# Performance work log

Measured on AMD Instinct MI355X. Metric: run time of the kernel, lower is better.

Reference implementation:

```python
import jax, jax.numpy as jnp
import numpy as np

EMBED_DIM = 1024
NUM_HEADS = 16
HEAD_DIM = EMBED_DIM // NUM_HEADS


def setup_inputs() -> dict:
    key = jax.random.key(0)
    k_x, k_wqkv, k_bqkv, k_wout, k_bout = jax.random.split(key, 5)
    scale = 1.0 / np.sqrt(EMBED_DIM)
    return {
        "x": jax.random.normal(k_x, (2, 2048, EMBED_DIM), dtype=jnp.float32),
        "W_qkv": jax.random.normal(k_wqkv, (3 * EMBED_DIM, EMBED_DIM), dtype=jnp.float32) * scale,
        "b_qkv": jax.random.normal(k_bqkv, (3 * EMBED_DIM,), dtype=jnp.float32) * scale,
        "W_out": jax.random.normal(k_wout, (EMBED_DIM, EMBED_DIM), dtype=jnp.float32) * scale,
        "b_out": jax.random.normal(k_bout, (EMBED_DIM,), dtype=jnp.float32) * scale,
    }


def reference(x, W_qkv, b_qkv, W_out, b_out):
    B, L, D = x.shape
    H, hd = NUM_HEADS, HEAD_DIM
    # fused QKV projection (torch Linear: x @ W.T + b)
    qkv = x @ W_qkv.T + b_qkv                      # [B, L, 3D]
    q, k, v = jnp.split(qkv, 3, axis=-1)           # each [B, L, D]
    # [B, L, D] -> [B, H, L, hd]
    q = q.reshape(B, L, H, hd).transpose(0, 2, 1, 3)
    k = k.reshape(B, L, H, hd).transpose(0, 2, 1, 3)
    v = v.reshape(B, L, H, hd).transpose(0, 2, 1, 3)
    attn = jnp.einsum("bhqd,bhkd->bhqk", q, k) / jnp.sqrt(jnp.float32(hd))
    attn = jax.nn.softmax(attn, axis=-1)           # [B, H, L, L]
    out = jnp.einsum("bhqk,bhkd->bhqd", attn, v)   # [B, H, L, hd]
    out = out.transpose(0, 2, 1, 3).reshape(B, L, D)
    return out @ W_out.T + b_out
```

## Files before the change

kernel.cpp:

```cpp
#include <hip/hip_runtime.h>
#include <hip/hip_bf16.h>

typedef __attribute__((ext_vector_type(8))) _Float16 f16x8;
typedef __attribute__((ext_vector_type(4))) _Float16 f16x4;
typedef __attribute__((ext_vector_type(2))) _Float16 f16x2;
typedef __attribute__((ext_vector_type(4))) float f32x4;
typedef __attribute__((ext_vector_type(16))) float f32x16;

__device__ __forceinline__ void gload16(const void* g, void* l) {
  __builtin_amdgcn_global_load_lds((const __attribute__((address_space(1))) void*)g,
                                   (__attribute__((address_space(3))) void*)l, 16, 0, 0);
}
__device__ __forceinline__ unsigned pk2(float a, float b) {
  f16x2 t;
  t[0] = (_Float16)a;
  t[1] = (_Float16)b;
  return __builtin_bit_cast(unsigned, t);
}

__global__ __launch_bounds__(256) void cast_all(const float* __restrict__ x,
                                                const float* __restrict__ wqkv,
                                                const float* __restrict__ wout,
                                                _Float16* __restrict__ xh,
                                                _Float16* __restrict__ wqkvh,
                                                _Float16* __restrict__ wouth) {
  const int i = (blockIdx.x * 256 + threadIdx.x) * 8;
  const float* s;
  _Float16* d;
  int off;
  if (i < 4194304) {
    s = x; d = xh; off = i;
  } else if (i < 7340032) {
    s = wqkv; d = wqkvh; off = i - 4194304;
  } else {
    s = wout; d = wouth; off = i - 7340032;
  }
  const float4 v0 = *reinterpret_cast<const float4*>(s + off);
  const float4 v1 = *reinterpret_cast<const float4*>(s + off + 4);
  f16x8 h;
  h[0] = (_Float16)v0.x; h[1] = (_Float16)v0.y; h[2] = (_Float16)v0.z; h[3] = (_Float16)v0.w;
  h[4] = (_Float16)v1.x; h[5] = (_Float16)v1.y; h[6] = (_Float16)v1.z; h[7] = (_Float16)v1.w;
  *reinterpret_cast<f16x8*>(d + off) = h;
}

template <int EPI>
__global__ __launch_bounds__(256) void gemm_bt(
    const _Float16* __restrict__ A, const _Float16* __restrict__ Bm,
    const float* __restrict__ bias, float* __restrict__ Cout,
    _Float16* __restrict__ Qo, _Float16* __restrict__ Ko, _Float16* __restrict__ Vto,
    int Ndim, int Kdim) {
  __shared__ __align__(16) _Float16 As[2][128 * 32];
  __shared__ __align__(16) _Float16 Bs[2][128 * 32];
  const int tid = threadIdx.x, lane = tid & 63, wave = tid >> 6;
  const int wm = wave >> 1, wn = wave & 1;
  const int m0 = blockIdx.y * 128, n0 = blockIdx.x * 128;
  const int row = lane & 15, kk = (lane >> 4) * 8;

  const int r0 = tid >> 2, c0 = (tid & 3) * 8;
  const int r1 = (256 + tid) >> 2, c1 = ((256 + tid) & 3) * 8;
  const _Float16* a0 = A + (size_t)(m0 + r0) * Kdim + c0;
  const _Float16* a1 = A + (size_t)(m0 + r1) * Kdim + c1;
  const _Float16* b0 = Bm + (size_t)(n0 + r0) * Kdim + c0;
  const _Float16* b1 = Bm + (size_t)(n0 + r1) * Kdim + c1;

  f32x4 acc[4][4];
#pragma unroll
  for (int i = 0; i < 4; ++i)
#pragma unroll
    for (int j = 0; j < 4; ++j)
#pragma unroll
      for (int q = 0; q < 4; ++q) acc[i][j][q] = 0.f;

  auto STAGE = [&](int bufi, int k0) {
    char* dA = (char*)&As[bufi][0] + (wave * 64) * 16;
    char* dB = (char*)&Bs[bufi][0] + (wave * 64) * 16;
    gload16(a0 + k0, dA);
    gload16(a1 + k0, dA + 4096);
    gload16(b0 + k0, dB);
    gload16(b1 + k0, dB + 4096);
  };

  STAGE(0, 0);
  asm volatile("s_waitcnt vmcnt(0)" ::: "memory");
  __syncthreads();

  for (int k0 = 0; k0 < Kdim; k0 += 32) {
    const int cur = (k0 >> 5) & 1;
    if (k0 + 32 < Kdim) STAGE(cur ^ 1, k0 + 32);
    f16x8 af[4], bf[4];
#pragma unroll
    for (int i = 0; i < 4; ++i)
      af[i] = *reinterpret_cast<const f16x8*>(&As[cur][(wm * 64 + i * 16 + row) * 32 + kk]);
#pragma unroll
    for (int j = 0; j < 4; ++j)
      bf[j] = *reinterpret_cast<const f16x8*>(&Bs[cur][(wn * 64 + j * 16 + row) * 32 + kk]);
#pragma unroll
    for (int i = 0; i < 4; ++i)
#pragma unroll
      for (int j = 0; j < 4; ++j)
        acc[i][j] = __builtin_amdgcn_mfma_f32_16x16x32_f16(af[i], bf[j], acc[i][j], 0, 0, 0);
    asm volatile("s_waitcnt vmcnt(0)" ::: "memory");
    __syncthreads();
  }

#pragma unroll
  for (int i = 0; i < 4; ++i) {
#pragma unroll
    for (int j = 0; j < 4; ++j) {
#pragma unroll
      for (int q = 0; q < 4; ++q) {
        const int gm = m0 + wm * 64 + i * 16 + (lane >> 4) * 4 + q;
        const int gn = n0 + wn * 64 + j * 16 + row;
        const float c = acc[i][j][q] + bias[gn];
        if (EPI == 1) {
          Cout[(size_t)gm * Ndim + gn] = c;
        } else {
          const int b = gm >> 11, l = gm & 2047;
          const int part = gn >> 10, dD = gn & 1023;
          const int h = dD >> 6, dd = dD & 63;
          const int bh = b * 16 + h;
          if (part == 0)
            Qo[((size_t)bh * 2048 + l) * 64 + dd] = (_Float16)(c * 0.1803368801f);
          else if (part == 1)
            Ko[((size_t)bh * 2048 + l) * 64 + dd] = (_Float16)c;
          else
            Vto[((size_t)bh * 64 + dd) * 2048 + l] = (_Float16)c;
        }
      }
    }
  }
}

__global__ __launch_bounds__(256, 2) void attn_fwd(const _Float16* __restrict__ Qh,
                                                   const _Float16* __restrict__ Kh,
                                                   const _Float16* __restrict__ Vth,
                                                   _Float16* __restrict__ AOh) {
  __shared__ __align__(16) uint4 KVs[2][1024];
  const int tid = threadIdx.x, lane = tid & 63, wave = tid >> 6;
  const int bid = blockIdx.x;
  const int bh = bid & 31, qb = bid >> 5;
  const int b = bh >> 4, h = bh & 15;
  const int q0 = qb * 128 + wave * 32;
  const _Float16* Qp = Qh + ((size_t)bh * 2048 + q0) * 64;
  const _Float16* Kp = Kh + (size_t)bh * 2048 * 64;
  const _Float16* Vp = Vth + (size_t)bh * 64 * 2048;
  const int r31 = lane & 31, hl = lane >> 5, r7 = lane & 7;

  const int kr0 = tid >> 3, ks0 = (tid & 7) ^ (kr0 & 7);
  const int kr1 = (256 + tid) >> 3, ks1 = ((256 + tid) & 7) ^ (kr1 & 7);
  const _Float16* ksrc0 = Kp + (size_t)kr0 * 64 + ks0 * 8;
  const _Float16* ksrc1 = Kp + (size_t)kr1 * 64 + ks1 * 8;
  const _Float16* vsrc0 = Vp + (size_t)kr0 * 2048 + ks0 * 8;
  const _Float16* vsrc1 = Vp + (size_t)kr1 * 2048 + ks1 * 8;

  f16x8 qf[4];
#pragma unroll
  for (int kd = 0; kd < 4; ++kd)
    qf[kd] = *reinterpret_cast<const f16x8*>(&Qp[r31 * 64 + kd * 16 + hl * 8]);

  f32x16 o0, o1;
#pragma unroll
  for (int i = 0; i < 16; ++i) { o0[i] = 0.f; o1[i] = 0.f; }
  float mrun = -3.0e38f, lsum = 0.f;

  auto STAGE = [&](uint4* base, int t) {
    gload16(ksrc0 + (size_t)t * 4096, base + wave * 64);
    gload16(ksrc1 + (size_t)t * 4096, base + 256 + wave * 64);
    gload16(vsrc0 + t * 64, base + 512 + wave * 64);
    gload16(vsrc1 + t * 64, base + 768 + wave * 64);
  };

  auto ITER = [&](int t, uint4* cur, uint4* nxt) {
    if (t < 31) STAGE(nxt, t + 1);
    const char* KB = (const char*)cur;
    const char* VB = (const char*)(cur + 512);

    f32x16 st[2];
    __builtin_amdgcn_s_setprio(1);
#pragma unroll
    for (int t32 = 0; t32 < 2; ++t32) {
#pragma unroll
      for (int i = 0; i < 16; ++i) st[t32][i] = 0.f;
#pragma unroll
      for (int kd = 0; kd < 4; ++kd) {
        const f16x8 kf = *reinterpret_cast<const f16x8*>(
            KB + (((t32 * 32 + r31) * 8 + ((kd * 2 + hl) ^ r7)) << 4));
        st[t32] = __builtin_amdgcn_mfma_f32_32x32x16_f16(kf, qf[kd], st[t32], 0, 0, 0);
      }
    }
    __builtin_amdgcn_s_setprio(0);

    f16x8 vf[2][2][2];
#pragma unroll
    for (int hh = 0; hh < 2; ++hh)
#pragma unroll
      for (int t32 = 0; t32 < 2; ++t32)
#pragma unroll
        for (int s = 0; s < 2; ++s)
          vf[hh][t32][s] = *reinterpret_cast<const f16x8*>(
              VB + (((hh * 32 + r31) * 8 + (((t32 * 2 + s) * 2 + hl) ^ r7)) << 4));

    float ma = fmaxf(st[0][0], st[0][1]);
    float mb = fmaxf(st[1][0], st[1][1]);
#pragma unroll
    for (int i = 2; i < 16; i += 2) {
      ma = fmaxf(fmaxf(st[0][i], st[0][i + 1]), ma);
      mb = fmaxf(fmaxf(st[1][i], st[1][i + 1]), mb);
    }
    const float mt = fmaxf(ma, mb);
    if (!__all(mt - mrun <= 11.f)) {
      const float mts = fmaxf(mt, __shfl_xor(mt, 32));
      const float mn = fmaxf(mrun, mts);
      const float al = exp2f(mrun - mn);
      lsum *= al;
#pragma unroll
      for (int i = 0; i < 16; ++i) { o0[i] *= al; o1[i] *= al; }
      mrun = mn;
    }
    float pr[32];
    float rs = 0.f;
#pragma unroll
    for (int i = 0; i < 16; ++i) {
      pr[i] = exp2f(st[0][i] - mrun);
      rs += pr[i];
    }
#pragma unroll
    for (int i = 0; i < 16; ++i) {
      pr[16 + i] = exp2f(st[1][i] - mrun);
      rs += pr[16 + i];
    }
    lsum += rs;

    __builtin_amdgcn_s_setprio(1);
#pragma unroll
    for (int t32 = 0; t32 < 2; ++t32) {
#pragma unroll
      for (int s = 0; s < 2; ++s) {
        const int bi = t32 * 16 + s * 8;
        const unsigned Aw = pk2(pr[bi + 0], pr[bi + 1]);
        const unsigned A2 = pk2(pr[bi + 2], pr[bi + 3]);
        const unsigned Bw = pk2(pr[bi + 4], pr[bi + 5]);
        const unsigned B2 = pk2(pr[bi + 6], pr[bi + 7]);
        const unsigned r1 = __shfl_xor(hl ? Aw : Bw, 32);
        const unsigned r2 = __shfl_xor(hl ? A2 : B2, 32);
        union { unsigned u[4]; f16x8 v; } pf;
        pf.u[0] = hl ? r1 : Aw;
        pf.u[1] = hl ? r2 : A2;
        pf.u[2] = hl ? Bw : r1;
        pf.u[3] = hl ? B2 : r2;
        o0 = __builtin_amdgcn_mfma_f32_32x32x16_f16(vf[0][t32][s], pf.v, o0, 0, 0, 0);
        o1 = __builtin_amdgcn_mfma_f32_32x32x16_f16(vf[1][t32][s], pf.v, o1, 0, 0, 0);
      }
    }
    __builtin_amdgcn_s_setprio(0);

    if (t < 31) {
      asm volatile("s_waitcnt vmcnt(0)" ::: "memory");
      __syncthreads();
    }
  };

  STAGE(KVs[0], 0);
  asm volatile("s_waitcnt vmcnt(0)" ::: "memory");
  __syncthreads();

  for (int tt = 0; tt < 16; ++tt) {
    ITER(2 * tt, KVs[0], KVs[1]);
    ITER(2 * tt + 1, KVs[1], KVs[0]);
  }

  const float ltot = lsum + __shfl_xor(lsum, 32);
  const float inv = 1.f / ltot;
  const size_t orow = (size_t)b * 2048 + q0 + r31;
#pragma unroll
  for (int hh = 0; hh < 2; ++hh) {
#pragma unroll
    for (int rr = 0; rr < 4; ++rr) {
      f16x4 c;
#pragma unroll
      for (int j = 0; j < 4; ++j)
        c[j] = (_Float16)((hh ? o1[rr * 4 + j] : o0[rr * 4 + j]) * inv);
      const int hd = 8 * rr + 4 * hl + 32 * hh;
      *reinterpret_cast<f16x4*>(&AOh[orow * 1024 + h * 64 + hd]) = c;
    }
  }
}

extern "C" void kernel_launch(void* const* d_in, const int* in_sizes, int n_in, void* d_out,
                              int out_size, void* d_ws, size_t ws_size, hipStream_t stream) {
  const float* x = (const float*)d_in[0];
  const float* Wqkv = (const float*)d_in[1];
  const float* bqkv = (const float*)d_in[2];
  const float* Wout = (const float*)d_in[3];
  const float* bout = (const float*)d_in[4];
  float* out = (float*)d_out;

  char* ws = (char*)d_ws;
  _Float16* xh = (_Float16*)(ws);
  _Float16* wqkvh = (_Float16*)(ws + 8388608);
  _Float16* wouth = (_Float16*)(ws + 14680064);
  _Float16* Qh = (_Float16*)(ws + 16777216);
  _Float16* Kh = (_Float16*)(ws + 25165824);
  _Float16* Vth = (_Float16*)(ws + 33554432);
  _Float16* AOh = (_Float16*)(ws + 41943040);

  cast_all<<<4096, 256, 0, stream>>>(x, Wqkv, Wout, xh, wqkvh, wouth);
  gemm_bt<0><<<dim3(24, 32), 256, 0, stream>>>(xh, wqkvh, bqkv, nullptr, Qh, Kh, Vth, 3072, 1024);
  attn_fwd<<<512, 256, 0, stream>>>(Qh, Kh, Vth, AOh);
  gemm_bt<1><<<dim3(8, 32), 256, 0, stream>>>(AOh, wouth, bout, out, nullptr, nullptr, nullptr,
                                              1024, 1024);
}
```

Measured before the change: 142.6 us.

## Fold running max into MFMA accumulator init, use native exp2/pkrtz, swizzle GEMM blocks

The attention score accumulator is initialised with the negated running max, so exponentiation needs no per-element subtraction, and the rescale branch subtracts the delta only when it triggers. Max and sum reductions become tree reductions to shorten dependency chains. exp2 and the fp16 packing now use the hardware builtins (round-toward-zero packing). The GEMM also remaps block IDs so neighbouring workgroups are spread across an 8-way interleave for better cache locality on the chiplet layout. The trade-offs are slightly different rounding from RTZ conversion and the lack of denormal handling in the raw exp2.

```diff
diff --git a/kernel.cpp b/kernel.cpp
--- a/kernel.cpp
+++ b/kernel.cpp
@@ -6,16 +6,29 @@
 typedef __attribute__((ext_vector_type(2))) _Float16 f16x2;
 typedef __attribute__((ext_vector_type(4))) float f32x4;
 typedef __attribute__((ext_vector_type(16))) float f32x16;
+typedef __attribute__((ext_vector_type(2))) __fp16 fp16v2;
 
 __device__ __forceinline__ void gload16(const void* g, void* l) {
   __builtin_amdgcn_global_load_lds((const __attribute__((address_space(1))) void*)g,
                                    (__attribute__((address_space(3))) void*)l, 16, 0, 0);
 }
+__device__ __forceinline__ float fexp2(float x) {
+#if __has_builtin(__builtin_amdgcn_exp2f)
+  return __builtin_amdgcn_exp2f(x);
+#else
+  return exp2f(x);
+#endif
+}
 __device__ __forceinline__ unsigned pk2(float a, float b) {
+#if __has_builtin(__builtin_amdgcn_cvt_pkrtz)
+  fp16v2 r = __builtin_amdgcn_cvt_pkrtz(a, b);
+  return __builtin_bit_cast(unsigned, r);
+#else
   f16x2 t;
   t[0] = (_Float16)a;
   t[1] = (_Float16)b;
   return __builtin_bit_cast(unsigned, t);
+#endif
 }
 
 __global__ __launch_bounds__(256) void cast_all(const float* __restrict__ x,
@@ -53,7 +66,10 @@
   __shared__ __align__(16) _Float16 Bs[2][128 * 32];
   const int tid = threadIdx.x, lane = tid & 63, wave = tid >> 6;
   const int wm = wave >> 1, wn = wave & 1;
-  const int m0 = blockIdx.y * 128, n0 = blockIdx.x * 128;
+  const int nwg = gridDim.x * gridDim.y;
+  int bidl = blockIdx.y * gridDim.x + blockIdx.x;
+  bidl = (bidl & 7) * (nwg >> 3) + (bidl >> 3);
+  const int m0 = (bidl / gridDim.x) * 128, n0 = (bidl % gridDim.x) * 128;
   const int row = lane & 15, kk = (lane >> 4) * 8;
 
   const int r0 = tid >> 2, c0 = (tid & 3) * 8;
@@ -161,7 +177,7 @@
   f32x16 o0, o1;
 #pragma unroll
   for (int i = 0; i < 16; ++i) { o0[i] = 0.f; o1[i] = 0.f; }
-  float mrun = -3.0e38f, lsum = 0.f;
+  float mrun = 0.f, lsum = 0.f;
 
   auto STAGE = [&](uint4* base, int t) {
     gload16(ksrc0 + (size_t)t * 4096, base + wave * 64);
@@ -175,12 +191,13 @@
     const char* KB = (const char*)cur;
     const char* VB = (const char*)(cur + 512);
 
+    const float negm = -mrun;
     f32x16 st[2];
     __builtin_amdgcn_s_setprio(1);
 #pragma unroll
     for (int t32 = 0; t32 < 2; ++t32) {
 #pragma unroll
-      for (int i = 0; i < 16; ++i) st[t32][i] = 0.f;
+      for (int i = 0; i < 16; ++i) st[t32][i] = negm;
 #pragma unroll
       for (int kd = 0; kd < 4; ++kd) {
         const f16x8 kf = *reinterpret_cast<const f16x8*>(
@@ -200,36 +217,42 @@
           vf[hh][t32][s] = *reinterpret_cast<const f16x8*>(
               VB + (((hh * 32 + r31) * 8 + (((t32 * 2 + s) * 2 + hl) ^ r7)) << 4));
 
-    float ma = fmaxf(st[0][0], st[0][1]);
-    float mb = fmaxf(st[1][0], st[1][1]);
-#pragma unroll
-    for (int i = 2; i < 16; i += 2) {
-      ma = fmaxf(fmaxf(st[0][i], st[0][i + 1]), ma);
-      mb = fmaxf(fmaxf(st[1][i], st[1][i + 1]), mb);
-    }
-    const float mt = fmaxf(ma, mb);
-    if (!__all(mt - mrun <= 11.f)) {
+    float m16[16];
+#pragma unroll
+    for (int i = 0; i < 16; ++i) m16[i] = fmaxf(st[0][i], st[1][i]);
+#pragma unroll
+    for (int w = 8; w; w >>= 1)
+#pragma unroll
+      for (int i = 0; i < 8; ++i)
+        if (i < w) m16[i] = fmaxf(m16[i], m16[i + w]);
+    const float mt = m16[0];
+    if (!__all(mt <= 11.f)) {
       const float mts = fmaxf(mt, __shfl_xor(mt, 32));
-      const float mn = fmaxf(mrun, mts);
-      const float al = exp2f(mrun - mn);
+      const float d = fmaxf(mts, 0.f);
+      const float al = fexp2(-d);
       lsum *= al;
 #pragma unroll
       for (int i = 0; i < 16; ++i) { o0[i] *= al; o1[i] *= al; }
-      mrun = mn;
+      mrun += d;
+#pragma unroll
+      for (int t32 = 0; t32 < 2; ++t32)
+#pragma unroll
+        for (int i = 0; i < 16; ++i) st[t32][i] -= d;
     }
     float pr[32];
-    float rs = 0.f;
-#pragma unroll
-    for (int i = 0; i < 16; ++i) {
-      pr[i] = exp2f(st[0][i] - mrun);
-      rs += pr[i];
-    }
-#pragma unroll
-    for (int i = 0; i < 16; ++i) {
-      pr[16 + i] = exp2f(st[1][i] - mrun);
-      rs += pr[16 + i];
-    }
-    lsum += rs;
+#pragma unroll
+    for (int i = 0; i < 16; ++i) pr[i] = fexp2(st[0][i]);
+#pragma unroll
+    for (int i = 0; i < 16; ++i) pr[16 + i] = fexp2(st[1][i]);
+    float s16[16];
+#pragma unroll
+    for (int i = 0; i < 16; ++i) s16[i] = pr[i] + pr[16 + i];
+#pragma unroll
+    for (int w = 8; w; w >>= 1)
+#pragma unroll
+      for (int i = 0; i < 8; ++i)
+        if (i < w) s16[i] += s16[i + w];
+    lsum += s16[0];
 
     __builtin_amdgcn_s_setprio(1);
 #pragma unroll
```

Result: faster. 126.9 us (-11.0%).
